# Kernel tuning notes

Hardware: AMD Instinct MI355X
Metric: run time of the kernel (lower is better)

The kernel has to match this reference:

```python
import jax, jax.numpy as jnp
import numpy as np

N_NODES = 10000
N_EDGES = 160000
N_FEAT = 512
HEADS = 8
HID = 128
OUT = 16


def setup_inputs() -> dict:
    key = jax.random.key(0)
    ks = jax.random.split(key, 16)
    inp = {
        'node_features': jax.random.normal(ks[0], (N_NODES, N_FEAT), jnp.float32),
        'edge_src': jax.random.randint(ks[1], (N_EDGES,), 0, N_NODES, jnp.int32),
        'edge_dst': jax.random.randint(ks[2], (N_EDGES,), 0, N_NODES, jnp.int32),
        # GAT layer params (scaled randn for numerical sanity)
        'W1': jax.random.normal(ks[3], (HEADS, HID, N_FEAT), jnp.float32) * 0.05,
        'a1': jax.random.normal(ks[4], (HEADS, 2 * HID), jnp.float32) * 0.05,
        'W2': jax.random.normal(ks[5], (HEADS, HID, HID), jnp.float32) * 0.05,
        'a2': jax.random.normal(ks[6], (HEADS, 2 * HID), jnp.float32) * 0.05,
        # MLP: LayerNorm(128) -> Linear(128,64) -> LeakyReLU -> Linear(64,16) -> LeakyReLU -> Linear(16,OUT) -> ReLU
        'ln_g': jnp.ones((HID,), jnp.float32),
        'ln_b': jnp.zeros((HID,), jnp.float32),
        'Wl1': jax.random.normal(ks[7], (64, HID), jnp.float32) * 0.05,
        'bl1': jnp.zeros((64,), jnp.float32),
        'Wl2': jax.random.normal(ks[8], (16, 64), jnp.float32) * 0.05,
        'bl2': jnp.zeros((16,), jnp.float32),
        'Wl3': jax.random.normal(ks[9], (OUT, 16), jnp.float32) * 0.05,
        'bl3': jnp.zeros((OUT,), jnp.float32),
    }
    return inp


def gat_layer(x, src, dst, W, a, n_nodes):
    # per-node, per-head projection: h[n,h,d]
    h = jnp.einsum('hdf,nf->nhd', W, x)
    # split attention vector: e_ij = a[:HID].h_i + a[HID:].h_j
    s_i = jnp.einsum('nhd,hd->nh', h, a[:, :HID])  # score contribution of target i
    s_j = jnp.einsum('nhd,hd->nh', h, a[:, HID:])  # score contribution of neighbor j
    e = jax.nn.leaky_relu(s_i[dst] + s_j[src])     # [E,H], negative_slope=0.01 (torch default)
    # segment softmax over edges grouped by dst
    m = jax.ops.segment_max(e, dst, num_segments=n_nodes)           # [N,H]
    m = jnp.where(jnp.isfinite(m), m, 0.0)
    ex = jnp.exp(e - m[dst])                                        # [E,H]
    denom = jax.ops.segment_sum(ex, dst, num_segments=n_nodes)      # [N,H]
    alpha = ex / jnp.where(denom > 0, denom, 1.0)[dst]              # [E,H]
    # scatter-accumulate weighted neighbor embeddings
    agg = jax.ops.segment_sum(alpha[:, :, None] * h[src], dst, num_segments=n_nodes)  # [N,H,HID]
    # average over heads, ELU (matches 1/attn_heads * attn_sum -> ELU)
    return jax.nn.elu(agg.mean(axis=1))  # [N,HID]


def reference(node_features, edge_src, edge_dst, W1, a1, W2, a2,
              ln_g, ln_b, Wl1, bl1, Wl2, bl2, Wl3, bl3):
    n = node_features.shape[0]
    emb1 = gat_layer(node_features, edge_src, edge_dst, W1, a1, n)
    emb2 = gat_layer(emb1, edge_src, edge_dst, W2, a2, n)
    g = emb2.mean(axis=0)  # [HID] graph embedding
    # MLP head (dropout = identity at inference)
    mu = g.mean()
    var = ((g - mu) ** 2).mean()
    gn = (g - mu) / jnp.sqrt(var + 1e-5) * ln_g + ln_b
    x = jax.nn.leaky_relu(Wl1 @ gn + bl1)
    x = jax.nn.leaky_relu(Wl2 @ x + bl2)
    return jax.nn.relu(Wl3 @ x + bl3)
```

## Files before the change

### kernel.cpp

```cpp
#include <hip/hip_runtime.h>
#include <math.h>

#define N_NODES 10000
#define N_EDGES 160000
#define N_FEAT  512
#define HEADS   8
#define HID     128

typedef __attribute__((ext_vector_type(8))) short bf16x8;
typedef __attribute__((ext_vector_type(4))) float f32x4;
typedef __attribute__((ext_vector_type(2))) float v2f;

__device__ inline unsigned short f2bf_rne(float f) {
  unsigned int u = __float_as_uint(f);
  unsigned int r = u + 0x7fffu + ((u >> 16) & 1u);
  return (unsigned short)(r >> 16);
}
__device__ inline float bf2f(unsigned int b) {
  return __uint_as_float(b << 16);
}

__device__ inline void split_body(const float* __restrict__ in,
                                  unsigned short* __restrict__ hi,
                                  unsigned short* __restrict__ lo,
                                  int R, int K8, int idx) {
  int r = idx & 15;
  int t = idx >> 4;
  int kq = t % K8;
  int rb = t / K8;
  int row = rb * 16 + r;
  float v[8] = {0.f, 0.f, 0.f, 0.f, 0.f, 0.f, 0.f, 0.f};
  if (row < R) {
    const float* p = in + (size_t)row * (K8 * 8) + kq * 8;
    float4 a = *(const float4*)p;
    float4 b = *(const float4*)(p + 4);
    v[0] = a.x; v[1] = a.y; v[2] = a.z; v[3] = a.w;
    v[4] = b.x; v[5] = b.y; v[6] = b.z; v[7] = b.w;
  }
  union { unsigned short u[8]; int4 v4; } H, L;
  #pragma unroll
  for (int e = 0; e < 8; ++e) {
    unsigned short hb_ = f2bf_rne(v[e]);
    H.u[e] = hb_;
    L.u[e] = f2bf_rne(v[e] - bf2f(hb_));
  }
  *(int4*)&hi[(size_t)idx * 8] = H.v4;
  *(int4*)&lo[(size_t)idx * 8] = L.v4;
}

__global__ __launch_bounds__(256)
void split_frag2(const float* __restrict__ in1, unsigned short* __restrict__ hi1,
                 unsigned short* __restrict__ lo1, int R1, int K81, int total1,
                 int nb1,
                 const float* __restrict__ in2, unsigned short* __restrict__ hi2,
                 unsigned short* __restrict__ lo2, int R2, int K82, int total2) {
  if ((int)blockIdx.x < nb1) {
    int idx = blockIdx.x * 256 + threadIdx.x;
    if (idx < total1) split_body(in1, hi1, lo1, R1, K81, idx);
  } else {
    int idx = (blockIdx.x - nb1) * 256 + threadIdx.x;
    if (idx < total2) split_body(in2, hi2, lo2, R2, K82, idx);
  }
}

__global__ __launch_bounds__(128, 3)
void gemm_frag(const unsigned short* __restrict__ Afh,
               const unsigned short* __restrict__ Afl,
               const unsigned short* __restrict__ Bfh,
               const unsigned short* __restrict__ Bfl,
               const float* __restrict__ avec,
               unsigned short* __restrict__ hb,
               float* __restrict__ si, float* __restrict__ sj,
               int M, int K) {
  __shared__ float rsi[64][2];
  __shared__ float rsj[64][2];
  int tid = threadIdx.x;
  int wave = tid >> 6, lane = tid & 63;
  int r = lane & 15, q = lane >> 4;

  int blk = blockIdx.x;
  int rr = blk & 7, gg = blk >> 3;
  int head = gg & 7;
  int mtile = (gg >> 3) * 8 + rr;
  int m0 = mtile * 64;
  int wn = wave * 64;
  int K8 = K >> 3;

  const bf16x8* pAh = (const bf16x8*)Afh;
  const bf16x8* pAl = (const bf16x8*)Afl;
  const bf16x8* pBh = (const bf16x8*)Bfh;
  const bf16x8* pBl = (const bf16x8*)Bfl;
  size_t rstep = (size_t)K8 * 16;
  size_t aidx = (size_t)(m0 >> 4) * rstep + (size_t)q * 16 + r;
  size_t bidx = (size_t)(head * 8 + (wn >> 4)) * rstep + (size_t)q * 16 + r;

  f32x4 acc[4][4] = {};

  for (int k0 = 0; k0 < K; k0 += 32, aidx += 64, bidx += 64) {
    bf16x8 ah[4], al[4], bh[4], bl[4];
    #pragma unroll
    for (int i = 0; i < 4; ++i) {
      ah[i] = pAh[aidx + i * rstep];
      al[i] = pAl[aidx + i * rstep];
      bh[i] = pBh[bidx + i * rstep];
      bl[i] = pBl[bidx + i * rstep];
    }
    #pragma unroll
    for (int i = 0; i < 4; ++i)
      #pragma unroll
      for (int j = 0; j < 4; ++j) {
        acc[i][j] = __builtin_amdgcn_mfma_f32_16x16x32_bf16(ah[i], bh[j], acc[i][j], 0, 0, 0);
        acc[i][j] = __builtin_amdgcn_mfma_f32_16x16x32_bf16(ah[i], bl[j], acc[i][j], 0, 0, 0);
        acc[i][j] = __builtin_amdgcn_mfma_f32_16x16x32_bf16(al[i], bh[j], acc[i][j], 0, 0, 0);
      }
  }

  const float* av = avec + (size_t)head * (2 * HID);
  float aiv[4], ajv[4];
  #pragma unroll
  for (int j = 0; j < 4; ++j) {
    int c = wn + j * 16 + r;
    aiv[j] = av[c];
    ajv[j] = av[HID + c];
  }
  #pragma unroll
  for (int i = 0; i < 4; ++i) {
    #pragma unroll
    for (int reg = 0; reg < 4; ++reg) {
      int lrow = i * 16 + q * 4 + reg;
      int row = m0 + lrow;
      float vsi = 0.f, vsj = 0.f;
      #pragma unroll
      for (int j = 0; j < 4; ++j) {
        float v = acc[i][j][reg];
        vsi = fmaf(v, aiv[j], vsi);
        vsj = fmaf(v, ajv[j], vsj);
        if (row < M)
          hb[((size_t)head * M + row) * HID + wn + j * 16 + r] = f2bf_rne(v);
      }
      #pragma unroll
      for (int o = 8; o >= 1; o >>= 1) {
        vsi += __shfl_xor(vsi, o);
        vsj += __shfl_xor(vsj, o);
      }
      if (r == 0) {
        rsi[lrow][wave] = vsi;
        rsj[lrow][wave] = vsj;
      }
    }
  }
  __syncthreads();
  if (tid < 64) {
    int row = m0 + tid;
    if (row < M) {
      si[(size_t)row * HEADS + head] = rsi[tid][0] + rsi[tid][1];
      sj[(size_t)row * HEADS + head] = rsj[tid][0] + rsj[tid][1];
    }
  }
}

__global__ void count_kernel(const int* __restrict__ dst, int* __restrict__ deg, int E) {
  int e = blockIdx.x * blockDim.x + threadIdx.x;
  if (e < E) atomicAdd(&deg[dst[e]], 1);
}

__global__ __launch_bounds__(1024)
void scan_kernel(const int* __restrict__ deg, int* __restrict__ off, int N) {
  __shared__ int sums[1024];
  const int PER = 10;
  int tid = threadIdx.x;
  int base = tid * PER;
  int loc[PER];
  int run = 0;
  #pragma unroll
  for (int j = 0; j < PER; ++j) {
    int v = (base + j < N) ? deg[base + j] : 0;
    run += v;
    loc[j] = run;
  }
  sums[tid] = run;
  __syncthreads();
  for (int o = 1; o < 1024; o <<= 1) {
    int v = (tid >= o) ? sums[tid - o] : 0;
    __syncthreads();
    sums[tid] += v;
    __syncthreads();
  }
  int ex = sums[tid] - run;
  if (tid == 0) off[0] = 0;
  #pragma unroll
  for (int j = 0; j < PER; ++j)
    if (base + j < N) off[base + j + 1] = ex + loc[j];
}

__global__ void fill_kernel(const int* __restrict__ src, const int* __restrict__ dst,
                            const int* __restrict__ off, int* __restrict__ cursor,
                            int* __restrict__ ssrc, int E) {
  int e = blockIdx.x * blockDim.x + threadIdx.x;
  if (e < E) {
    int d = dst[e];
    int p = atomicAdd(&cursor[d], 1);
    ssrc[off[d] + p] = src[e];
  }
}

__global__ __launch_bounds__(512)
void gat_aggregate7(const unsigned short* __restrict__ hb,
                    const float* __restrict__ si, const float* __restrict__ sj,
                    const int* __restrict__ off, const int* __restrict__ ssrc,
                    unsigned short* __restrict__ aggb, int N) {
  __shared__ int2 prs[8][64];
  int head = blockIdx.x & 7;
  int wv = threadIdx.x >> 6;
  int n = (blockIdx.x >> 3) * 8 + wv;
  int lane = threadIdx.x & 63;
  int grp = lane >> 4;
  int l = lane & 15;
  const unsigned short* hbase = hb + (size_t)head * N * HID;
  int begin = off[n], end = off[n + 1];
  int deg = end - begin;
  int dmin = deg < 64 ? deg : 64;
  float s_i = si[n * HEADS + head];

  int src0 = 0;
  float sc0 = -INFINITY;
  if (lane < deg) {
    src0 = ssrc[begin + lane];
    float t = s_i + sj[src0 * HEADS + head];
    sc0 = t > 0.f ? t : 0.01f * t;
  }
  float m = sc0;
  for (int e2 = 64 + lane; e2 < deg; e2 += 64) {
    int s = ssrc[begin + e2];
    float t = s_i + sj[s * HEADS + head];
    t = t > 0.f ? t : 0.01f * t;
    m = fmaxf(m, t);
  }
  #pragma unroll
  for (int o = 1; o <= 32; o <<= 1) m = fmaxf(m, __shfl_xor(m, o));

  float w0 = (lane < deg) ? expf(sc0 - m) : 0.f;
  float den = w0;
  for (int e2 = 64 + lane; e2 < deg; e2 += 64) {
    int s = ssrc[begin + e2];
    float t = s_i + sj[s * HEADS + head];
    t = t > 0.f ? t : 0.01f * t;
    den += expf(t - m);
  }
  #pragma unroll
  for (int o = 1; o <= 32; o <<= 1) den += __shfl_xor(den, o);

  prs[wv][lane] = make_int2(src0, __float_as_int(w0));
  __asm__ volatile("s_waitcnt lgkmcnt(0)" ::: "memory");

  v2f a01 = {0.f, 0.f}, a23 = {0.f, 0.f}, a45 = {0.f, 0.f}, a67 = {0.f, 0.f};

  for (int e0 = 0; e0 < dmin; e0 += 16) {
    float we[4];
    int se[4];
    #pragma unroll
    for (int u = 0; u < 4; ++u) {
      int e = e0 + u * 4 + grp;
      int2 p = prs[wv][e];
      se[u] = p.x;
      we[u] = __int_as_float(p.y);
    }
    int4 pv[4];
    #pragma unroll
    for (int u = 0; u < 4; ++u)
      pv[u] = *(const int4*)&hbase[(size_t)se[u] * HID + l * 8];
    #pragma unroll
    for (int u = 0; u < 4; ++u) {
      v2f w2 = {we[u], we[u]};
      int4 p = pv[u];
      v2f t0 = {bf2f((unsigned)p.x & 0xffffu), __uint_as_float((unsigned)p.x & 0xffff0000u)};
      v2f t1 = {bf2f((unsigned)p.y & 0xffffu), __uint_as_float((unsigned)p.y & 0xffff0000u)};
      v2f t2 = {bf2f((unsigned)p.z & 0xffffu), __uint_as_float((unsigned)p.z & 0xffff0000u)};
      v2f t3 = {bf2f((unsigned)p.w & 0xffffu), __uint_as_float((unsigned)p.w & 0xffff0000u)};
      a01 += w2 * t0;
      a23 += w2 * t1;
      a45 += w2 * t2;
      a67 += w2 * t3;
    }
  }
  for (int e2 = 64; e2 < deg; e2 += 4) {
    int e = e2 + grp;
    bool valid = e < deg;
    int s = ssrc[valid ? begin + e : begin];
    float t = s_i + sj[s * HEADS + head];
    t = t > 0.f ? t : 0.01f * t;
    float wu = valid ? expf(t - m) : 0.f;
    v2f w2 = {wu, wu};
    int4 p = *(const int4*)&hbase[(size_t)s * HID + l * 8];
    v2f t0 = {bf2f((unsigned)p.x & 0xffffu), __uint_as_float((unsigned)p.x & 0xffff0000u)};
    v2f t1 = {bf2f((unsigned)p.y & 0xffffu), __uint_as_float((unsigned)p.y & 0xffff0000u)};
    v2f t2 = {bf2f((unsigned)p.z & 0xffffu), __uint_as_float((unsigned)p.z & 0xffff0000u)};
    v2f t3 = {bf2f((unsigned)p.w & 0xffffu), __uint_as_float((unsigned)p.w & 0xffff0000u)};
    a01 += w2 * t0; a23 += w2 * t1; a45 += w2 * t2; a67 += w2 * t3;
  }

  #pragma unroll
  for (int o = 16; o <= 32; o <<= 1) {
    a01.x += __shfl_xor(a01.x, o); a01.y += __shfl_xor(a01.y, o);
    a23.x += __shfl_xor(a23.x, o); a23.y += __shfl_xor(a23.y, o);
    a45.x += __shfl_xor(a45.x, o); a45.y += __shfl_xor(a45.y, o);
    a67.x += __shfl_xor(a67.x, o); a67.y += __shfl_xor(a67.y, o);
  }

  if (grp == 0) {
    float inv = den > 0.f ? 1.0f / den : 0.f;
    union { unsigned short u[8]; int4 v4; } P;
    P.u[0] = f2bf_rne(a01.x * inv); P.u[1] = f2bf_rne(a01.y * inv);
    P.u[2] = f2bf_rne(a23.x * inv); P.u[3] = f2bf_rne(a23.y * inv);
    P.u[4] = f2bf_rne(a45.x * inv); P.u[5] = f2bf_rne(a45.y * inv);
    P.u[6] = f2bf_rne(a67.x * inv); P.u[7] = f2bf_rne(a67.y * inv);
    *(int4*)&aggb[((size_t)head * N + n) * HID + l * 8] = P.v4;
  }
}

__global__ __launch_bounds__(256)
void headmean_frag_w2(const unsigned short* __restrict__ aggb,
                      unsigned short* __restrict__ hiA, unsigned short* __restrict__ loA,
                      int N, int nbHM,
                      const float* __restrict__ W2, unsigned short* __restrict__ hiB,
                      unsigned short* __restrict__ loB, int totalB) {
  if ((int)blockIdx.x >= nbHM) {
    int idx = (blockIdx.x - nbHM) * 256 + threadIdx.x;
    if (idx < totalB) split_body(W2, hiB, loB, HEADS * HID, 16, idx);
    return;
  }
  int idx = blockIdx.x * 256 + threadIdx.x;
  int total = ((N + 15) / 16) * 256;
  if (idx >= total) return;
  int r = idx & 15;
  int kq = (idx >> 4) & 15;
  int rb = idx >> 8;
  int n = rb * 16 + r;
  float s[8] = {0.f, 0.f, 0.f, 0.f, 0.f, 0.f, 0.f, 0.f};
  if (n < N) {
    #pragma unroll
    for (int hh = 0; hh < HEADS; ++hh) {
      int4 pv = *(const int4*)&aggb[((size_t)hh * N + n) * HID + kq * 8];
      s[0] += bf2f((unsigned)pv.x & 0xffffu);
      s[1] += __uint_as_float((unsigned)pv.x & 0xffff0000u);
      s[2] += bf2f((unsigned)pv.y & 0xffffu);
      s[3] += __uint_as_float((unsigned)pv.y & 0xffff0000u);
      s[4] += bf2f((unsigned)pv.z & 0xffffu);
      s[5] += __uint_as_float((unsigned)pv.z & 0xffff0000u);
      s[6] += bf2f((unsigned)pv.w & 0xffffu);
      s[7] += __uint_as_float((unsigned)pv.w & 0xffff0000u);
    }
  }
  union { unsigned short u[8]; int4 v4; } H, L;
  #pragma unroll
  for (int e = 0; e < 8; ++e) {
    float v = s[e] * (1.0f / HEADS);
    v = v > 0.f ? v : (expf(v) - 1.0f);
    unsigned short hb_ = f2bf_rne(v);
    H.u[e] = hb_;
    L.u[e] = f2bf_rne(v - bf2f(hb_));
  }
  *(int4*)&hiA[(size_t)idx * 8] = H.v4;
  *(int4*)&loA[(size_t)idx * 8] = L.v4;
}

__global__ __launch_bounds__(256)
void headmean_pool(const unsigned short* __restrict__ aggb, float* __restrict__ g,
                   int N) {
  __shared__ float sm[16][128];
  int t = threadIdx.x;
  int nl = t >> 4, dg = t & 15;
  int n = blockIdx.x * 16 + nl;
  float v[8] = {0.f, 0.f, 0.f, 0.f, 0.f, 0.f, 0.f, 0.f};
  if (n < N) {
    #pragma unroll
    for (int hh = 0; hh < HEADS; ++hh) {
      int4 pv = *(const int4*)&aggb[((size_t)hh * N + n) * HID + dg * 8];
      v[0] += bf2f((unsigned)pv.x & 0xffffu);
      v[1] += __uint_as_float((unsigned)pv.x & 0xffff0000u);
      v[2] += bf2f((unsigned)pv.y & 0xffffu);
      v[3] += __uint_as_float((unsigned)pv.y & 0xffff0000u);
      v[4] += bf2f((unsigned)pv.z & 0xffffu);
      v[5] += __uint_as_float((unsigned)pv.z & 0xffff0000u);
      v[6] += bf2f((unsigned)pv.w & 0xffffu);
      v[7] += __uint_as_float((unsigned)pv.w & 0xffff0000u);
    }
    #pragma unroll
    for (int e = 0; e < 8; ++e) {
      float x = v[e] * (1.0f / HEADS);
      v[e] = x > 0.f ? x : (expf(x) - 1.0f);
    }
  }
  #pragma unroll
  for (int e = 0; e < 8; ++e) sm[nl][dg * 8 + e] = v[e];
  __syncthreads();
  if (t < 128) {
    float s = 0.f;
    #pragma unroll
    for (int nn = 0; nn < 16; ++nn) s += sm[nn][t];
    atomicAdd(&g[t], s);
  }
}

__global__ __launch_bounds__(128)
void mlp_kernel(const float* __restrict__ g, const float* __restrict__ ln_g,
                const float* __restrict__ ln_b, const float* __restrict__ Wl1,
                const float* __restrict__ bl1, const float* __restrict__ Wl2,
                const float* __restrict__ bl2, const float* __restrict__ Wl3,
                const float* __restrict__ bl3, float* __restrict__ out, float invN) {
  __shared__ float red[128];
  __shared__ float gn[128];
  __shared__ float x1[64];
  __shared__ float x2[16];
  int t = threadIdx.x;
  float gg = g[t] * invN;
  red[t] = gg;
  __syncthreads();
  for (int o = 64; o > 0; o >>= 1) {
    if (t < o) red[t] += red[t + o];
    __syncthreads();
  }
  float mu = red[0] * (1.0f / HID);
  __syncthreads();
  float dv = gg - mu;
  red[t] = dv * dv;
  __syncthreads();
  for (int o = 64; o > 0; o >>= 1) {
    if (t < o) red[t] += red[t + o];
    __syncthreads();
  }
  float var = red[0] * (1.0f / HID);
  gn[t] = dv / sqrtf(var + 1e-5f) * ln_g[t] + ln_b[t];
  __syncthreads();
  if (t < 64) {
    float s = bl1[t];
    for (int k = 0; k < 128; ++k) s += Wl1[t * 128 + k] * gn[k];
    x1[t] = s > 0.f ? s : 0.01f * s;
  }
  __syncthreads();
  if (t < 16) {
    float s = bl2[t];
    for (int k = 0; k < 64; ++k) s += Wl2[t * 64 + k] * x1[k];
    x2[t] = s > 0.f ? s : 0.01f * s;
  }
  __syncthreads();
  if (t < 16) {
    float s = bl3[t];
    for (int k = 0; k < 16; ++k) s += Wl3[t * 16 + k] * x2[k];
    out[t] = s > 0.f ? s : 0.f;
  }
}

extern "C" void kernel_launch(void* const* d_in, const int* in_sizes, int n_in,
                              void* d_out, int out_size, void* d_ws, size_t ws_size,
                              hipStream_t stream) {
  const float* x    = (const float*)d_in[0];
  const int*   esrc = (const int*)d_in[1];
  const int*   edst = (const int*)d_in[2];
  const float* W1   = (const float*)d_in[3];
  const float* a1   = (const float*)d_in[4];
  const float* W2   = (const float*)d_in[5];
  const float* a2   = (const float*)d_in[6];
  const float* ln_g = (const float*)d_in[7];
  const float* ln_b = (const float*)d_in[8];
  const float* Wl1  = (const float*)d_in[9];
  const float* bl1  = (const float*)d_in[10];
  const float* Wl2  = (const float*)d_in[11];
  const float* bl2  = (const float*)d_in[12];
  const float* Wl3  = (const float*)d_in[13];
  const float* bl3  = (const float*)d_in[14];
  float* out = (float*)d_out;

  const int RBPAD = 640;

  unsigned short* aggb = (unsigned short*)d_ws;
  float* si   = (float*)(aggb + (size_t)N_NODES * HEADS * HID);
  float* sj   = si + N_NODES * HEADS;
  float* g    = sj + N_NODES * HEADS;
  int*   deg  = (int*)(g + 128);
  int*   cur  = deg + N_NODES;
  int*   off  = cur + N_NODES;
  int*   ssrc = off + 10004;
  unsigned short* Afh = (unsigned short*)(ssrc + N_EDGES);
  unsigned short* Afl = Afh + (size_t)RBPAD * 64 * 128;
  unsigned short* Bfh = Afl + (size_t)RBPAD * 64 * 128;
  unsigned short* Bfl = Bfh + (size_t)64 * 64 * 128;
  unsigned short* hb  = Bfl + (size_t)64 * 64 * 128;

  hipMemsetAsync(g, 0, 128 * sizeof(float) + 2 * N_NODES * sizeof(int), stream);
  count_kernel<<<(N_EDGES + 255) / 256, 256, 0, stream>>>(edst, deg, N_EDGES);
  scan_kernel<<<1, 1024, 0, stream>>>(deg, off, N_NODES);
  fill_kernel<<<(N_EDGES + 255) / 256, 256, 0, stream>>>(esrc, edst, off, cur, ssrc, N_EDGES);

  int gemmGrid = 160 * HEADS;
  int aggGrid = (N_NODES / 8) * 8;

  {
    int totalA = RBPAD * 64 * 16;
    int nbA = (totalA + 255) / 256;
    int totalB = 64 * 64 * 16;
    int nbB = (totalB + 255) / 256;
    split_frag2<<<nbA + nbB, 256, 0, stream>>>(x, Afh, Afl, N_NODES, 64, totalA, nbA,
                                               W1, Bfh, Bfl, HEADS * HID, 64, totalB);
    gemm_frag<<<gemmGrid, 128, 0, stream>>>(Afh, Afl, Bfh, Bfl, a1, hb,
                                            si, sj, N_NODES, N_FEAT);
  }
  gat_aggregate7<<<aggGrid, 512, 0, stream>>>(hb, si, sj, off, ssrc, aggb, N_NODES);
  {
    int nbHM = ((N_NODES + 15) / 16 * 256 + 255) / 256;
    int totalB = 64 * 16 * 16;
    int nbB = (totalB + 255) / 256;
    headmean_frag_w2<<<nbHM + nbB, 256, 0, stream>>>(aggb, Afh, Afl, N_NODES, nbHM,
                                                     W2, Bfh, Bfl, totalB);
  }

  gemm_frag<<<gemmGrid, 128, 0, stream>>>(Afh, Afl, Bfh, Bfl, a2, hb,
                                          si, sj, N_NODES, HID);
  gat_aggregate7<<<aggGrid, 512, 0, stream>>>(hb, si, sj, off, ssrc, aggb, N_NODES);

  headmean_pool<<<(N_NODES + 15) / 16, 256, 0, stream>>>(aggb, g, N_NODES);
  mlp_kernel<<<1, 128, 0, stream>>>(g, ln_g, ln_b, Wl1, bl1, Wl2, bl2, Wl3, bl3,
                                    out, 1.0f / N_NODES);
}
```

Before: 302.6 us.

## Fuse degree count into split kernel, head-major scores, fast exp

The edge degree-count kernel is folded into the split_frag2 launch as extra blocks, removing one kernel launch. The per-node attention scores si/sj switch from node-major to head-major layout, so gathers of sj for one head read a single contiguous array. expf is replaced with __expf in the softmax and ELU paths, which is cheaper but slightly less accurate.

```diff
diff --git a/kernel.cpp b/kernel.cpp
--- a/kernel.cpp
+++ b/kernel.cpp
@@ -53,13 +53,18 @@
                  unsigned short* __restrict__ lo1, int R1, int K81, int total1,
                  int nb1,
                  const float* __restrict__ in2, unsigned short* __restrict__ hi2,
-                 unsigned short* __restrict__ lo2, int R2, int K82, int total2) {
+                 unsigned short* __restrict__ lo2, int R2, int K82, int total2,
+                 int nb2,
+                 const int* __restrict__ edst, int* __restrict__ deg, int E) {
   if ((int)blockIdx.x < nb1) {
     int idx = blockIdx.x * 256 + threadIdx.x;
     if (idx < total1) split_body(in1, hi1, lo1, R1, K81, idx);
-  } else {
+  } else if ((int)blockIdx.x < nb1 + nb2) {
     int idx = (blockIdx.x - nb1) * 256 + threadIdx.x;
     if (idx < total2) split_body(in2, hi2, lo2, R2, K82, idx);
+  } else {
+    int e = (blockIdx.x - nb1 - nb2) * 256 + threadIdx.x;
+    if (e < E) atomicAdd(&deg[edst[e]], 1);
   }
 }
 
@@ -153,15 +158,10 @@
   if (tid < 64) {
     int row = m0 + tid;
     if (row < M) {
-      si[(size_t)row * HEADS + head] = rsi[tid][0] + rsi[tid][1];
-      sj[(size_t)row * HEADS + head] = rsj[tid][0] + rsj[tid][1];
-    }
-  }
-}
-
-__global__ void count_kernel(const int* __restrict__ dst, int* __restrict__ deg, int E) {
-  int e = blockIdx.x * blockDim.x + threadIdx.x;
-  if (e < E) atomicAdd(&deg[dst[e]], 1);
+      si[(size_t)head * M + row] = rsi[tid][0] + rsi[tid][1];
+      sj[(size_t)head * M + row] = rsj[tid][0] + rsj[tid][1];
+    }
+  }
 }
 
 __global__ __launch_bounds__(1024)
@@ -217,35 +217,36 @@
   int grp = lane >> 4;
   int l = lane & 15;
   const unsigned short* hbase = hb + (size_t)head * N * HID;
+  const float* sjh = sj + (size_t)head * N;
   int begin = off[n], end = off[n + 1];
   int deg = end - begin;
   int dmin = deg < 64 ? deg : 64;
-  float s_i = si[n * HEADS + head];
+  float s_i = si[(size_t)head * N + n];
 
   int src0 = 0;
   float sc0 = -INFINITY;
   if (lane < deg) {
     src0 = ssrc[begin + lane];
-    float t = s_i + sj[src0 * HEADS + head];
+    float t = s_i + sjh[src0];
     sc0 = t > 0.f ? t : 0.01f * t;
   }
   float m = sc0;
   for (int e2 = 64 + lane; e2 < deg; e2 += 64) {
     int s = ssrc[begin + e2];
-    float t = s_i + sj[s * HEADS + head];
+    float t = s_i + sjh[s];
     t = t > 0.f ? t : 0.01f * t;
     m = fmaxf(m, t);
   }
   #pragma unroll
   for (int o = 1; o <= 32; o <<= 1) m = fmaxf(m, __shfl_xor(m, o));
 
-  float w0 = (lane < deg) ? expf(sc0 - m) : 0.f;
+  float w0 = (lane < deg) ? __expf(sc0 - m) : 0.f;
   float den = w0;
   for (int e2 = 64 + lane; e2 < deg; e2 += 64) {
     int s = ssrc[begin + e2];
-    float t = s_i + sj[s * HEADS + head];
+    float t = s_i + sjh[s];
     t = t > 0.f ? t : 0.01f * t;
-    den += expf(t - m);
+    den += __expf(t - m);
   }
   #pragma unroll
   for (int o = 1; o <= 32; o <<= 1) den += __shfl_xor(den, o);
@@ -287,9 +288,9 @@
     int e = e2 + grp;
     bool valid = e < deg;
     int s = ssrc[valid ? begin + e : begin];
-    float t = s_i + sj[s * HEADS + head];
+    float t = s_i + sjh[s];
     t = t > 0.f ? t : 0.01f * t;
-    float wu = valid ? expf(t - m) : 0.f;
+    float wu = valid ? __expf(t - m) : 0.f;
     v2f w2 = {wu, wu};
     int4 p = *(const int4*)&hbase[(size_t)s * HID + l * 8];
     v2f t0 = {bf2f((unsigned)p.x & 0xffffu), __uint_as_float((unsigned)p.x & 0xffff0000u)};
@@ -355,7 +356,7 @@
   #pragma unroll
   for (int e = 0; e < 8; ++e) {
     float v = s[e] * (1.0f / HEADS);
-    v = v > 0.f ? v : (expf(v) - 1.0f);
+    v = v > 0.f ? v : (__expf(v) - 1.0f);
     unsigned short hb_ = f2bf_rne(v);
     H.u[e] = hb_;
     L.u[e] = f2bf_rne(v - bf2f(hb_));
@@ -388,7 +389,7 @@
     #pragma unroll
     for (int e = 0; e < 8; ++e) {
       float x = v[e] * (1.0f / HEADS);
-      v[e] = x > 0.f ? x : (expf(x) - 1.0f);
+      v[e] = x > 0.f ? x : (__expf(x) - 1.0f);
     }
   }
   #pragma unroll
@@ -488,9 +489,6 @@
   unsigned short* hb  = Bfl + (size_t)64 * 64 * 128;
 
   hipMemsetAsync(g, 0, 128 * sizeof(float) + 2 * N_NODES * sizeof(int), stream);
-  count_kernel<<<(N_EDGES + 255) / 256, 256, 0, stream>>>(edst, deg, N_EDGES);
-  scan_kernel<<<1, 1024, 0, stream>>>(deg, off, N_NODES);
-  fill_kernel<<<(N_EDGES + 255) / 256, 256, 0, stream>>>(esrc, edst, off, cur, ssrc, N_EDGES);
 
   int gemmGrid = 160 * HEADS;
   int aggGrid = (N_NODES / 8) * 8;
@@ -500,11 +498,17 @@
     int nbA = (totalA + 255) / 256;
     int totalB = 64 * 64 * 16;
     int nbB = (totalB + 255) / 256;
-    split_frag2<<<nbA + nbB, 256, 0, stream>>>(x, Afh, Afl, N_NODES, 64, totalA, nbA,
-                                               W1, Bfh, Bfl, HEADS * HID, 64, totalB);
-    gemm_frag<<<gemmGrid, 128, 0, stream>>>(Afh, Afl, Bfh, Bfl, a1, hb,
-                                            si, sj, N_NODES, N_FEAT);
-  }
+    int nbE = (N_EDGES + 255) / 256;
+    split_frag2<<<nbA + nbB + nbE, 256, 0, stream>>>(
+        x, Afh, Afl, N_NODES, 64, totalA, nbA,
+        W1, Bfh, Bfl, HEADS * HID, 64, totalB, nbB,
+        edst, deg, N_EDGES);
+  }
+  scan_kernel<<<1, 1024, 0, stream>>>(deg, off, N_NODES);
+  fill_kernel<<<(N_EDGES + 255) / 256, 256, 0, stream>>>(esrc, edst, off, cur, ssrc, N_EDGES);
+
+  gemm_frag<<<gemmGrid, 128, 0, stream>>>(Afh, Afl, Bfh, Bfl, a1, hb,
+                                          si, sj, N_NODES, N_FEAT);
   gat_aggregate7<<<aggGrid, 512, 0, stream>>>(hb, si, sj, off, ssrc, aggb, N_NODES);
   {
     int nbHM = ((N_NODES + 15) / 16 * 256 + 255) / 256;
```

New measurement: 299.6 us. No clear change (-1.0%).
